# Performance work log

Hardware: AMD Instinct MI355X
Metric: run time of the kernel (lower is better)

## Reference

```python
import jax, jax.numpy as jnp
import numpy as np

B, N, F, S, OUT = 8, 12000, 128, 16, 128

def setup_inputs() -> dict:
    key = jax.random.key(0)
    k1, k2, k3, k4 = jax.random.split(key, 4)
    x = jax.random.normal(k1, (B, N, F), dtype=jnp.float32)
    # Linear(in_c*spiral_size, out_c): weight [out, in], bias [out]
    bound = 1.0 / np.sqrt(F * S)
    W = jax.random.uniform(k2, (OUT, F * S), dtype=jnp.float32, minval=-bound, maxval=bound)
    b = jax.random.uniform(k3, (OUT,), dtype=jnp.float32, minval=-bound, maxval=bound)
    spiral_adj = jax.random.randint(k4, (1, N, S), 0, N, dtype=jnp.int32)
    zero_padding = jnp.ones((1, N, 1), dtype=jnp.float32)
    return {"x": x, "W": W, "b": b, "spiral_adj": spiral_adj, "zero_padding": zero_padding}

def reference(x, W, b, spiral_adj, zero_padding):
    # x: [B, N, F]; spiral_adj: [1, N, S] vertex indices shared across batch
    idx = spiral_adj[0]                         # [N, S]
    spirals = x[:, idx, :]                      # [B, N, S, F] gather along vertex dim
    bsz, npts, s, f = spirals.shape
    spirals = spirals.reshape(bsz, npts, s * f)  # [B, N, S*F]
    out = jnp.einsum('bnk,ok->bno', spirals, W) + b  # [B, N, OUT]
    out = jax.nn.relu(out)
    return out * zero_padding
```

## Files before the change

### kernel.cpp

```cpp
#include <hip/hip_runtime.h>

#define BATCH 8
#define NPTS  12000
#define FDIM  128
#define SDIM  16
#define ODIM  128
#define KDIM  (SDIM * FDIM)
#define MTOT  (BATCH * NPTS)

#define BM 128
#define BK 64

#define NTILES 94
#define XELEMS (BATCH * NPTS * FDIM)
#define WELEMS (ODIM * KDIM)
#define XBYTES ((size_t)XELEMS * 2)
#define WBYTES ((size_t)WELEMS * 2)
#define XN4    (XELEMS / 4)
#define WN4    (WELEMS / 4)

typedef __bf16 bf16x4 __attribute__((ext_vector_type(4)));
typedef __bf16 bf16x8 __attribute__((ext_vector_type(8)));
typedef float  f32x4  __attribute__((ext_vector_type(4)));
typedef float  f32x8  __attribute__((ext_vector_type(8)));

#define AS1(p) ((const __attribute__((address_space(1))) void*)(p))
#define AS3(p) ((__attribute__((address_space(3))) void*)(p))

__global__ __launch_bounds__(256)
void cvt_f32_bf16(const float* __restrict__ x, const float* __restrict__ W,
                  __bf16* __restrict__ xb, __bf16* __restrict__ Wb) {
    int i = blockIdx.x * blockDim.x + threadIdx.x;
    const int stride = gridDim.x * blockDim.x;
    for (; i < XN4 + WN4; i += stride) {
        const float* src; __bf16* dst; int j;
        if (i < XN4) { src = x; dst = xb; j = i; }
        else         { src = W; dst = Wb; j = i - XN4; }
        const float4 v = reinterpret_cast<const float4*>(src)[j];
        bf16x4 h;
        h[0] = (__bf16)v.x; h[1] = (__bf16)v.y;
        h[2] = (__bf16)v.z; h[3] = (__bf16)v.w;
        reinterpret_cast<bf16x4*>(dst)[j] = h;
    }
}

__global__ __launch_bounds__(256, 2)
void spiral_gemm_bf16(const __bf16* __restrict__ xb,
                      const __bf16* __restrict__ Wb,
                      const float*  __restrict__ bias,
                      const int*    __restrict__ idx,
                      const float*  __restrict__ zp,
                      float*        __restrict__ out)
{
    __shared__ __bf16 As[2][BM * BK];
    __shared__ __bf16 Ws[2][ODIM * BK];
    __shared__ int    idxS[BM * SDIM];

    const int tid   = threadIdx.x;
    const int wave  = tid >> 6;
    const int lane  = tid & 63;
    const int batch = blockIdx.x & 7;
    const int n0    = (blockIdx.x >> 3) * BM;

    const int lrow8 = lane >> 3;
    const int clog  = (lane & 7) ^ lrow8;

    const __bf16* xbase = xb + (size_t)batch * (NPTS * FDIM);

    {
        const int row  = tid >> 1, half = tid & 1;
        const int n    = n0 + row;
        const int nrow = n < NPTS ? n : NPTS - 1;
        const int4* s4 = reinterpret_cast<const int4*>(idx + nrow * SDIM + half * 8);
        int4* d4       = reinterpret_cast<int4*>(&idxS[row * SDIM + half * 8]);
        d4[0] = s4[0];
        d4[1] = s4[1];
    }
    __syncthreads();

    int rrow[4];
#pragma unroll
    for (int p = 0; p < 4; ++p) rrow[p] = (p * 4 + wave) * 8 + lrow8;

    int gCur[4], gNext[4];
#pragma unroll
    for (int p = 0; p < 4; ++p) gCur[p] = idxS[rrow[p] * SDIM + 0];

    auto issue = [&](int buf, int kt, const int* g) {
        const int f0 = (kt & 1) * BK;
#pragma unroll
        for (int p = 0; p < 4; ++p) {
            const int r0 = (p * 4 + wave) * 8;
            const __bf16* ga = xbase + (size_t)g[p] * FDIM + f0 + clog * 8;
            __builtin_amdgcn_global_load_lds(AS1(ga), AS3(&As[buf][r0 * BK]), 16, 0, 0);
            const __bf16* gw = Wb + (size_t)(r0 + lrow8) * KDIM + kt * BK + clog * 8;
            __builtin_amdgcn_global_load_lds(AS1(gw), AS3(&Ws[buf][r0 * BK]), 16, 0, 0);
        }
    };

    f32x4 acc[4][4];
#pragma unroll
    for (int i = 0; i < 4; ++i)
#pragma unroll
        for (int j = 0; j < 4; ++j)
            acc[i][j] = f32x4{0.f, 0.f, 0.f, 0.f};

    const int wm   = (wave >> 1) * 64;
    const int wn   = (wave & 1) * 64;
    const int lrow = lane & 15;
    const int quad = lane >> 4;

    auto compute = [&](int buf) {
#pragma unroll
        for (int kk = 0; kk < 2; ++kk) {
            const int ph = (kk * 4 + quad) ^ (lrow & 7);
            bf16x8 a[4], b[4];
#pragma unroll
            for (int i = 0; i < 4; ++i)
                a[i] = *reinterpret_cast<const bf16x8*>(
                    &As[buf][(wm + i * 16 + lrow) * BK + ph * 8]);
#pragma unroll
            for (int j = 0; j < 4; ++j)
                b[j] = *reinterpret_cast<const bf16x8*>(
                    &Ws[buf][(wn + j * 16 + lrow) * BK + ph * 8]);
#pragma unroll
            for (int i = 0; i < 4; ++i)
#pragma unroll
                for (int j = 0; j < 4; ++j)
                    acc[i][j] = __builtin_amdgcn_mfma_f32_16x16x32_bf16(
                        a[i], b[j], acc[i][j], 0, 0, 0);
        }
    };

    issue(0, 0, gCur);

    for (int t = 0; t < 16; ++t) {
        issue(1, 2 * t + 1, gCur);
        asm volatile("s_waitcnt vmcnt(8)" ::: "memory");
        asm volatile("s_barrier" ::: "memory");
        if (t < 15) {
#pragma unroll
            for (int p = 0; p < 4; ++p)
                gNext[p] = idxS[rrow[p] * SDIM + t + 1];
        }
        compute(0);
        asm volatile("s_barrier" ::: "memory");

        if (t < 15) {
            issue(0, 2 * t + 2, gNext);
            asm volatile("s_waitcnt vmcnt(8)" ::: "memory");
        } else {
            asm volatile("s_waitcnt vmcnt(0)" ::: "memory");
        }
        asm volatile("s_barrier" ::: "memory");
        compute(1);
        asm volatile("s_barrier" ::: "memory");
#pragma unroll
        for (int p = 0; p < 4; ++p) gCur[p] = gNext[p];
    }

#pragma unroll
    for (int i = 0; i < 4; ++i) {
#pragma unroll
        for (int r = 0; r < 4; ++r) {
            const int row = wm + i * 16 + quad * 4 + r;
            const int n   = n0 + row;
            if (n < NPTS) {
                const float z = zp[n];
                float* orow   = out + ((size_t)batch * NPTS + n) * ODIM;
#pragma unroll
                for (int j = 0; j < 4; ++j) {
                    const int col = wn + j * 16 + lrow;
                    float v = acc[i][j][r] + bias[col];
                    v = fmaxf(v, 0.f);
                    orow[col] = v * z;
                }
            }
        }
    }
}

#define LDA 72
__global__ __launch_bounds__(256, 2)
void spiral_gemm_fp32(const float* __restrict__ x, const float* __restrict__ W,
                      const float* __restrict__ bias, const int* __restrict__ idx,
                      const float* __restrict__ zp, float* __restrict__ out)
{
    __shared__ __bf16 Asf[BM * LDA];
    __shared__ __bf16 Wsf[ODIM * LDA];
    const int tid = threadIdx.x, wave = tid >> 6, lane = tid & 63;
    const int m0 = blockIdx.x * BM;
    const int srow = tid >> 3, schunk = tid & 7;
    int a_n[4]; const float* a_xb[4];
#pragma unroll
    for (int p = 0; p < 4; ++p) {
        int m = m0 + srow + p * 32, bb = m / NPTS;
        a_n[p] = m - bb * NPTS; a_xb[p] = x + (size_t)bb * (NPTS * FDIM);
    }
    f32x4 acc[4][4];
#pragma unroll
    for (int i = 0; i < 4; ++i)
#pragma unroll
        for (int j = 0; j < 4; ++j) acc[i][j] = f32x4{0.f,0.f,0.f,0.f};
    const int wm = (wave >> 1) * 64, wn = (wave & 1) * 64;
    const int lrow = lane & 15, quad = lane >> 4;
    for (int kt = 0; kt < KDIM / BK; ++kt) {
        const int s = kt >> 1, f0 = (kt & 1) * BK;
        __syncthreads();
#pragma unroll
        for (int p = 0; p < 4; ++p) {
            const int r = srow + p * 32;
            const int g = idx[a_n[p] * SDIM + s];
            const f32x8 v = *reinterpret_cast<const f32x8*>(
                a_xb[p] + (size_t)g * FDIM + f0 + schunk * 8);
            bf16x8 h;
#pragma unroll
            for (int e = 0; e < 8; ++e) h[e] = (__bf16)v[e];
            *reinterpret_cast<bf16x8*>(&Asf[r * LDA + schunk * 8]) = h;
            const f32x8 w = *reinterpret_cast<const f32x8*>(
                W + (size_t)r * KDIM + kt * BK + schunk * 8);
            bf16x8 hw;
#pragma unroll
            for (int e = 0; e < 8; ++e) hw[e] = (__bf16)w[e];
            *reinterpret_cast<bf16x8*>(&Wsf[r * LDA + schunk * 8]) = hw;
        }
        __syncthreads();
#pragma unroll
        for (int kk = 0; kk < 2; ++kk) {
            const int koff = kk * 32 + quad * 8;
            bf16x8 a[4], b[4];
#pragma unroll
            for (int i = 0; i < 4; ++i)
                a[i] = *reinterpret_cast<const bf16x8*>(&Asf[(wm + i*16 + lrow)*LDA + koff]);
#pragma unroll
            for (int j = 0; j < 4; ++j)
                b[j] = *reinterpret_cast<const bf16x8*>(&Wsf[(wn + j*16 + lrow)*LDA + koff]);
#pragma unroll
            for (int i = 0; i < 4; ++i)
#pragma unroll
                for (int j = 0; j < 4; ++j)
                    acc[i][j] = __builtin_amdgcn_mfma_f32_16x16x32_bf16(a[i], b[j], acc[i][j], 0,0,0);
        }
    }
#pragma unroll
    for (int i = 0; i < 4; ++i)
#pragma unroll
        for (int r = 0; r < 4; ++r) {
            const int row = wm + i * 16 + quad * 4 + r;
            const int m = m0 + row, bb = m / NPTS, nnn = m - bb * NPTS;
            const float z = zp[nnn];
            float* orow = out + (size_t)m * ODIM;
#pragma unroll
            for (int j = 0; j < 4; ++j) {
                const int col = wn + j * 16 + lrow;
                float v = acc[i][j][r] + bias[col];
                orow[col] = fmaxf(v, 0.f) * z;
            }
        }
}

extern "C" void kernel_launch(void* const* d_in, const int* in_sizes, int n_in,
                              void* d_out, int out_size, void* d_ws, size_t ws_size,
                              hipStream_t stream) {
    const float* x    = (const float*)d_in[0];
    const float* W    = (const float*)d_in[1];
    const float* bias = (const float*)d_in[2];
    const int*   idx  = (const int*)d_in[3];
    const float* zp   = (const float*)d_in[4];
    float*       out  = (float*)d_out;

    if (ws_size >= XBYTES + WBYTES) {
        __bf16* xb = (__bf16*)d_ws;
        __bf16* Wb = (__bf16*)((char*)d_ws + XBYTES);
        cvt_f32_bf16<<<dim3(1024), dim3(256), 0, stream>>>(x, W, xb, Wb);
        spiral_gemm_bf16<<<dim3(BATCH * NTILES), dim3(256), 0, stream>>>(
            xb, Wb, bias, idx, zp, out);
    } else {
        spiral_gemm_fp32<<<dim3(MTOT / BM), dim3(256), 0, stream>>>(
            x, W, bias, idx, zp, out);
    }
}
```

Before: 162.2 us.

## Split A and W DMA issue, stagger W loads mid-compute, add MFMA priority

The combined gather-plus-weight load is split into separate A and W DMA batches. Each W batch for the next buffer is now issued halfway through the current buffer's compute, between its two k-sub-steps, and the wait thresholds are retuned to vmcnt(4). MFMA blocks are wrapped in s_setprio to favour math issue. The intent is to overlap memory traffic with MFMA work more finely, at the cost of extra barriers and more fragile waitcnt bookkeeping.

```diff
diff --git a/kernel.cpp b/kernel.cpp
--- a/kernel.cpp
+++ b/kernel.cpp
@@ -86,77 +86,93 @@
 #pragma unroll
     for (int p = 0; p < 4; ++p) gCur[p] = idxS[rrow[p] * SDIM + 0];
 
-    auto issue = [&](int buf, int kt, const int* g) {
-        const int f0 = (kt & 1) * BK;
+    const int wm   = (wave >> 1) * 64;
+    const int wn   = (wave & 1) * 64;
+    const int lrow = lane & 15;
+    const int quad = lane >> 4;
+
+    f32x4 acc[4][4];
+#pragma unroll
+    for (int i = 0; i < 4; ++i)
+#pragma unroll
+        for (int j = 0; j < 4; ++j)
+            acc[i][j] = f32x4{0.f, 0.f, 0.f, 0.f};
+
+    auto dmaA4 = [&](int buf, int f0, const int* g) {
 #pragma unroll
         for (int p = 0; p < 4; ++p) {
             const int r0 = (p * 4 + wave) * 8;
             const __bf16* ga = xbase + (size_t)g[p] * FDIM + f0 + clog * 8;
             __builtin_amdgcn_global_load_lds(AS1(ga), AS3(&As[buf][r0 * BK]), 16, 0, 0);
-            const __bf16* gw = Wb + (size_t)(r0 + lrow8) * KDIM + kt * BK + clog * 8;
+        }
+    };
+    auto dmaW4 = [&](int buf, int ktn) {
+#pragma unroll
+        for (int p = 0; p < 4; ++p) {
+            const int r0 = (p * 4 + wave) * 8;
+            const __bf16* gw = Wb + (size_t)(r0 + lrow8) * KDIM + ktn * BK + clog * 8;
             __builtin_amdgcn_global_load_lds(AS1(gw), AS3(&Ws[buf][r0 * BK]), 16, 0, 0);
         }
     };
 
-    f32x4 acc[4][4];
-#pragma unroll
-    for (int i = 0; i < 4; ++i)
+    auto compute_kk = [&](int buf, int kk) {
+        const int ph = (kk * 4 + quad) ^ (lrow & 7);
+        bf16x8 a[4], b[4];
+#pragma unroll
+        for (int i = 0; i < 4; ++i)
+            a[i] = *reinterpret_cast<const bf16x8*>(
+                &As[buf][(wm + i * 16 + lrow) * BK + ph * 8]);
 #pragma unroll
         for (int j = 0; j < 4; ++j)
-            acc[i][j] = f32x4{0.f, 0.f, 0.f, 0.f};
-
-    const int wm   = (wave >> 1) * 64;
-    const int wn   = (wave & 1) * 64;
-    const int lrow = lane & 15;
-    const int quad = lane >> 4;
-
-    auto compute = [&](int buf) {
-#pragma unroll
-        for (int kk = 0; kk < 2; ++kk) {
-            const int ph = (kk * 4 + quad) ^ (lrow & 7);
-            bf16x8 a[4], b[4];
-#pragma unroll
-            for (int i = 0; i < 4; ++i)
-                a[i] = *reinterpret_cast<const bf16x8*>(
-                    &As[buf][(wm + i * 16 + lrow) * BK + ph * 8]);
+            b[j] = *reinterpret_cast<const bf16x8*>(
+                &Ws[buf][(wn + j * 16 + lrow) * BK + ph * 8]);
+        __builtin_amdgcn_s_setprio(1);
+#pragma unroll
+        for (int i = 0; i < 4; ++i)
 #pragma unroll
             for (int j = 0; j < 4; ++j)
-                b[j] = *reinterpret_cast<const bf16x8*>(
-                    &Ws[buf][(wn + j * 16 + lrow) * BK + ph * 8]);
-#pragma unroll
-            for (int i = 0; i < 4; ++i)
-#pragma unroll
-                for (int j = 0; j < 4; ++j)
-                    acc[i][j] = __builtin_amdgcn_mfma_f32_16x16x32_bf16(
-                        a[i], b[j], acc[i][j], 0, 0, 0);
-        }
+                acc[i][j] = __builtin_amdgcn_mfma_f32_16x16x32_bf16(
+                    a[i], b[j], acc[i][j], 0, 0, 0);
+        __builtin_amdgcn_s_setprio(0);
     };
 
-    issue(0, 0, gCur);
-
-    for (int t = 0; t < 16; ++t) {
-        issue(1, 2 * t + 1, gCur);
-        asm volatile("s_waitcnt vmcnt(8)" ::: "memory");
+    dmaA4(0, 0, gCur);
+    dmaW4(0, 0);
+
+    for (int u = 0; u < 16; ++u) {
+        dmaA4(1, BK, gCur);
+        asm volatile("s_waitcnt vmcnt(4)" ::: "memory");
         asm volatile("s_barrier" ::: "memory");
-        if (t < 15) {
+        compute_kk(0, 0);
+        asm volatile("s_barrier" ::: "memory");
+        dmaW4(1, 2 * u + 1);
+        if (u < 15) {
 #pragma unroll
             for (int p = 0; p < 4; ++p)
-                gNext[p] = idxS[rrow[p] * SDIM + t + 1];
-        }
-        compute(0);
+                gNext[p] = idxS[rrow[p] * SDIM + u + 1];
+        }
+        compute_kk(0, 1);
         asm volatile("s_barrier" ::: "memory");
 
-        if (t < 15) {
-            issue(0, 2 * t + 2, gNext);
-            asm volatile("s_waitcnt vmcnt(8)" ::: "memory");
+        if (u < 15) {
+            dmaA4(0, 0, gNext);
+            asm volatile("s_waitcnt vmcnt(4)" ::: "memory");
+            asm volatile("s_barrier" ::: "memory");
+            compute_kk(1, 0);
+            asm volatile("s_barrier" ::: "memory");
+            dmaW4(0, 2 * u + 2);
+            compute_kk(1, 1);
+            asm volatile("s_barrier" ::: "memory");
+#pragma unroll
+            for (int p = 0; p < 4; ++p) gCur[p] = gNext[p];
         } else {
             asm volatile("s_waitcnt vmcnt(0)" ::: "memory");
-        }
-        asm volatile("s_barrier" ::: "memory");
-        compute(1);
-        asm volatile("s_barrier" ::: "memory");
-#pragma unroll
-        for (int p = 0; p < 4; ++p) gCur[p] = gNext[p];
+            asm volatile("s_barrier" ::: "memory");
+            compute_kk(1, 0);
+            asm volatile("s_barrier" ::: "memory");
+            compute_kk(1, 1);
+            asm volatile("s_barrier" ::: "memory");
+        }
     }
 
 #pragma unroll
```

Result: slower. 169.2 us (+4.3%).
